# Kernel tuning notes

Hardware: AMD Instinct MI355X
Metric: run time of the kernel (lower is better)

## Reference

```python
import jax, jax.numpy as jnp
import numpy as np

N = 50000      # nodes
E = 400000     # edges
IN = 128       # in_channels
HID = 64       # hidden_channels (per head)
H = 4          # heads
OUT = 10       # classes
G = 64         # graphs in batch


def setup_inputs() -> dict:
    key = jax.random.key(0)
    ks = jax.random.split(key, 32)
    s = 0.05
    inp = {
        "x": jax.random.normal(ks[0], (N, IN), dtype=jnp.float32),
        "edge_index": jax.random.randint(ks[1], (2, E), 0, N, dtype=jnp.int32),
        "batch": jnp.sort(jax.random.randint(ks[2], (N,), 0, G, dtype=jnp.int32)),
    }
    # TransformerConv layer 1 params (in=IN -> heads*HID)
    d1 = H * HID
    inp["Wq1"] = jax.random.normal(ks[3], (IN, d1)) * s
    inp["bq1"] = jnp.zeros((d1,), jnp.float32)
    inp["Wk1"] = jax.random.normal(ks[4], (IN, d1)) * s
    inp["bk1"] = jnp.zeros((d1,), jnp.float32)
    inp["Wv1"] = jax.random.normal(ks[5], (IN, d1)) * s
    inp["bv1"] = jnp.zeros((d1,), jnp.float32)
    inp["Ws1"] = jax.random.normal(ks[6], (IN, d1)) * s   # root/skip weight
    inp["bs1"] = jnp.zeros((d1,), jnp.float32)
    # TransformerConv layer 2 params (in=H*HID -> heads*HID)
    inp["Wq2"] = jax.random.normal(ks[7], (d1, d1)) * s
    inp["bq2"] = jnp.zeros((d1,), jnp.float32)
    inp["Wk2"] = jax.random.normal(ks[8], (d1, d1)) * s
    inp["bk2"] = jnp.zeros((d1,), jnp.float32)
    inp["Wv2"] = jax.random.normal(ks[9], (d1, d1)) * s
    inp["bv2"] = jnp.zeros((d1,), jnp.float32)
    inp["Ws2"] = jax.random.normal(ks[10], (d1, d1)) * s
    inp["bs2"] = jnp.zeros((d1,), jnp.float32)
    # final classifier
    inp["Wl"] = jax.random.normal(ks[11], (d1, OUT)) * s
    inp["bl"] = jnp.zeros((OUT,), jnp.float32)
    return inp


def transformer_conv(x, src, dst, Wq, bq, Wk, bk, Wv, bv, Ws, bs):
    """PyG TransformerConv (concat=True, root_weight=True, beta=None, eval mode).
    src = edge_index[0] (source j), dst = edge_index[1] (target i).
    """
    n = x.shape[0]
    q = (x @ Wq + bq).reshape(n, H, HID)
    k = (x @ Wk + bk).reshape(n, H, HID)
    v = (x @ Wv + bv).reshape(n, H, HID)
    # per-edge attention logits [E, H]
    alpha = jnp.einsum('ehc,ehc->eh', q[dst], k[src]) / np.sqrt(HID).astype(np.float32)
    # scatter-softmax over incoming edges of each target node
    amax = jax.ops.segment_max(alpha, dst, num_segments=n)           # [N, H], -inf for isolated
    ex = jnp.exp(alpha - amax[dst])                                   # [E, H]
    denom = jax.ops.segment_sum(ex, dst, num_segments=n) + 1e-16      # [N, H]
    w = ex / denom[dst]                                               # normalized alpha [E, H]
    # scatter-sum aggregation of weighted values
    out = jax.ops.segment_sum(w[:, :, None] * v[src], dst, num_segments=n)  # [N, H, HID]
    out = out.reshape(n, H * HID)
    return out + (x @ Ws + bs)  # root/skip connection


def reference(x, edge_index, batch,
              Wq1, bq1, Wk1, bk1, Wv1, bv1, Ws1, bs1,
              Wq2, bq2, Wk2, bk2, Wv2, bv2, Ws2, bs2,
              Wl, bl):
    src, dst = edge_index[0], edge_index[1]
    h = jax.nn.elu(transformer_conv(x, src, dst, Wq1, bq1, Wk1, bk1, Wv1, bv1, Ws1, bs1))
    h = jax.nn.elu(transformer_conv(h, src, dst, Wq2, bq2, Wk2, bk2, Wv2, bv2, Ws2, bs2))
    # global mean pool per graph
    sums = jax.ops.segment_sum(h, batch, num_segments=G)              # [G, H*HID]
    cnt = jax.ops.segment_sum(jnp.ones((h.shape[0],), h.dtype), batch, num_segments=G)
    pooled = sums / jnp.maximum(cnt, 1.0)[:, None]
    logits = pooled @ Wl + bl
    return jax.nn.log_softmax(logits, axis=-1)
```

## Files before the change

### kernel.cpp

```cpp
#include <hip/hip_runtime.h>
#include <math.h>

constexpr int NN   = 50000;
constexpr int NE   = 400000;
constexpr int INC  = 128;
constexpr int NH   = 4;
constexpr int D1   = 256;
constexpr int D4   = 1024;
constexpr int NOUT = 10;
constexpr int NG   = 64;
constexpr int NB_SCAN = (NN + 255) / 256;


typedef __attribute__((ext_vector_type(8))) short bf16x8;
typedef __attribute__((ext_vector_type(4))) float f32x4;
typedef __attribute__((ext_vector_type(2))) float f32x2;

__device__ __forceinline__ short f2b(float f) {
  union { float f; unsigned int i; } v; v.f = f;
  unsigned int x = v.i;
  return (short)((x + 0x7FFFu + ((x >> 16) & 1u)) >> 16);
}
__device__ __forceinline__ float b2f(short u) {
  union { unsigned int i; float f; } v; v.i = ((unsigned int)(unsigned short)u) << 16;
  return v.f;
}
__device__ __forceinline__ float4 ld4b(const short* p) {
  short4 u = *(const short4*)p;
  return make_float4(b2f(u.x), b2f(u.y), b2f(u.z), b2f(u.w));
}
__device__ __forceinline__ int cvt_pk_bf16(float lo, float hi) {
  int r;
  asm volatile("v_cvt_pk_bf16_f32 %0, %1, %2" : "=v"(r) : "v"(lo), "v"(hi));
  return r;
}
__device__ __forceinline__ int pk_fp8x4(float a, float b, float c, float d) {
  int v = __builtin_amdgcn_cvt_pk_fp8_f32(a, b, 0, false);
  v = __builtin_amdgcn_cvt_pk_fp8_f32(c, d, v, true);
  return v;
}

__device__ __forceinline__ void gld_lds16(const short* g, short* l) {
  __builtin_amdgcn_global_load_lds(
      (const __attribute__((address_space(1))) unsigned int*)g,
      (__attribute__((address_space(3))) unsigned int*)l, 16, 0, 0);
}

constexpr int CVT_XB  = (NN * INC / 4 + 255) / 256;
constexpr int CVT_WTB = 48;
constexpr int CVT_BB  = 8;
constexpr int CVT_DB  = (NN + 255) / 256;
constexpr int CVT_FB  = 1;
constexpr int CVT_SB  = (NG * D1 + 255) / 256;

__global__ void cvt_all_k(const float* __restrict__ x, short* __restrict__ Xb,
    const float* __restrict__ Wq1, const float* __restrict__ Wk1,
    const float* __restrict__ Wv1, const float* __restrict__ Ws1,
    const float* __restrict__ Wq2, const float* __restrict__ Wk2,
    const float* __restrict__ Wv2, const float* __restrict__ Ws2,
    short* __restrict__ Wtc1, short* __restrict__ Wtc2,
    const float* __restrict__ bq1, const float* __restrict__ bk1,
    const float* __restrict__ bv1, const float* __restrict__ bs1,
    const float* __restrict__ bq2, const float* __restrict__ bk2,
    const float* __restrict__ bv2, const float* __restrict__ bs2,
    float* __restrict__ bc1, float* __restrict__ bc2,
    int* __restrict__ deg, unsigned int* __restrict__ desc,
    float* __restrict__ sums) {
  const int b = blockIdx.x;
  const int t = threadIdx.x;
  if (b < CVT_XB) {
    int i = (b * 256 + t) * 4;
    if (i >= NN * INC) return;
    float4 v = *(const float4*)(x + i);
    short4 o; o.x = f2b(v.x); o.y = f2b(v.y); o.z = f2b(v.z); o.w = f2b(v.w);
    *(short4*)(Xb + i) = o;
  } else if (b < CVT_XB + CVT_WTB) {
    const int w = b - CVT_XB;
    const bool l1 = (w < 16);
    const int mat   = l1 ? (w >> 2) : ((w - 16) >> 3);
    const int panel = l1 ? (w & 3)  : ((w - 16) & 7);
    const int K = l1 ? INC : D1;
    const int k0 = panel * 32;
    const float* Wm[8] = {Wq1, Wk1, Wv1, Ws1, Wq2, Wk2, Wv2, Ws2};
    const float* W = Wm[(l1 ? 0 : 4) + mat];
    short* Wt = l1 ? Wtc1 : Wtc2;
    int row;
    if (mat == 0)      row = t;
    else if (mat == 3) row = 768 + t;
    else               row = 256 + (t >> 2) * 8 + ((mat == 2) ? 4 : 0) + (t & 3);
    int4 pk[4];
    short* ps = (short*)pk;
#pragma unroll
    for (int kk = 0; kk < 32; ++kk)
      ps[kk] = f2b(W[(size_t)(k0 + kk) * D1 + t]);
#pragma unroll
    for (int j = 0; j < 4; ++j)
      *(int4*)(Wt + (size_t)row * K + k0 + j * 8) = pk[j];
  } else if (b < CVT_XB + CVT_WTB + CVT_BB) {
    int i = (b - CVT_XB - CVT_WTB) * 256 + t;
    if (i >= 2 * D4) return;
    int row = i & (D4 - 1);
    const float* bq = (i < D4) ? bq1 : bq2;
    const float* bk = (i < D4) ? bk1 : bk2;
    const float* bv = (i < D4) ? bv1 : bv2;
    const float* bs = (i < D4) ? bs1 : bs2;
    float v;
    if (row < 256) v = bq[row];
    else if (row < 768) {
      int j = row - 256, grp = j >> 3, off = j & 7;
      int ch = grp * 4 + (off & 3);
      v = (off < 4) ? bk[ch] : bv[ch];
    } else v = bs[row - 768];
    ((i < D4) ? bc1 : bc2)[row] = v;
  } else if (b < CVT_XB + CVT_WTB + CVT_BB + CVT_DB) {
    int i = (b - CVT_XB - CVT_WTB - CVT_BB) * 256 + t;
    if (i < NN) deg[i] = 0;
  } else if (b < CVT_XB + CVT_WTB + CVT_BB + CVT_DB + CVT_FB) {
    if (t < NB_SCAN) desc[t] = 0u;
  } else {
    int i = (b - CVT_XB - CVT_WTB - CVT_BB - CVT_DB - CVT_FB) * 256 + t;
    if (i < NG * D1) sums[i] = 0.f;
  }
}

__global__ void deg_count(const int* __restrict__ dst, int* __restrict__ deg) {
  int e = (blockIdx.x * 256 + threadIdx.x) * 4;
  if (e + 3 < NE) {
    const int4 d = *(const int4*)(dst + e);
    atomicAdd(&deg[d.x], 1);
    atomicAdd(&deg[d.y], 1);
    atomicAdd(&deg[d.z], 1);
    atomicAdd(&deg[d.w], 1);
  } else {
    for (; e < NE; ++e) atomicAdd(&deg[dst[e]], 1);
  }
}

__global__ __launch_bounds__(256) void scan_k(const int* __restrict__ deg,
    const int* __restrict__ batch, unsigned int* __restrict__ desc,
    int* __restrict__ rowstart, int* __restrict__ cursor, int* __restrict__ gb) {
  const int b = blockIdx.x;
  const int t = threadIdx.x;
  if (b == NB_SCAN) {
    if (t > NG) return;
    int lo = 0, hi = NN;
    while (lo < hi) {
      int mid = (lo + hi) >> 1;
      if (batch[mid] < t) lo = mid + 1; else hi = mid;
    }
    gb[t] = lo;
    return;
  }
  __shared__ int sh[256];
  __shared__ int base_s;
  const int i = b * 256 + t;
  const int v = (i < NN) ? deg[i] : 0;
  sh[t] = v;
  __syncthreads();
  for (int off = 1; off < 256; off <<= 1) {
    int o = (t >= off) ? sh[t - off] : 0;
    __syncthreads();
    sh[t] += o;
    __syncthreads();
  }
  const int incl = sh[t];
  const int aggr = sh[255];
  if (t == 0)
    __hip_atomic_store(&desc[b], ((unsigned int)aggr << 2) | (b == 0 ? 2u : 1u),
                       __ATOMIC_RELEASE, __HIP_MEMORY_SCOPE_AGENT);
  if (b == 0) {
    if (t == 0) base_s = 0;
  } else if (t < 64) {
    int base = 0;
    int j = b - 1;
    for (;;) {
      const int idx = j - t;
      const unsigned int d = (idx >= 0)
          ? __hip_atomic_load(&desc[idx], __ATOMIC_ACQUIRE,
                              __HIP_MEMORY_SCOPE_AGENT)
          : 2u;
      const unsigned int st = d & 3u;
      const unsigned long long m_incl = __ballot(st == 2u);
      const unsigned long long m_inv  = __ballot(st == 0u);
      const int fi = m_incl ? (__ffsll((unsigned long long)m_incl) - 1) : 64;
      const int fv = m_inv  ? (__ffsll((unsigned long long)m_inv ) - 1) : 64;
      if (fi < fv) {
        int contrib = (t <= fi) ? (int)(d >> 2) : 0;
#pragma unroll
        for (int off = 1; off < 64; off <<= 1) contrib += __shfl_xor(contrib, off, 64);
        base += contrib;
        break;
      } else if (fv == 64) {
        int contrib = (int)(d >> 2);
#pragma unroll
        for (int off = 1; off < 64; off <<= 1) contrib += __shfl_xor(contrib, off, 64);
        base += contrib;
        j -= 64;
      } else {
        __builtin_amdgcn_s_sleep(1);
      }
    }
    if (t == 0) {
      __hip_atomic_store(&desc[b], ((unsigned int)(base + aggr) << 2) | 2u,
                         __ATOMIC_RELEASE, __HIP_MEMORY_SCOPE_AGENT);
      base_s = base;
    }
  }
  __syncthreads();
  const int excl = base_s + incl - v;
  if (i <= NN) rowstart[i] = excl;
  if (i < NN)  cursor[i]   = excl;
}

__global__ void scatter_k(const int* __restrict__ src, const int* __restrict__ dst,
    int* __restrict__ cursor, int* __restrict__ esrc) {
  int e = (blockIdx.x * 256 + threadIdx.x) * 4;
  if (e + 3 < NE) {
    const int4 s4 = *(const int4*)(src + e);
    const int4 d4 = *(const int4*)(dst + e);
    esrc[atomicAdd(&cursor[d4.x], 1)] = s4.x;
    esrc[atomicAdd(&cursor[d4.y], 1)] = s4.y;
    esrc[atomicAdd(&cursor[d4.z], 1)] = s4.z;
    esrc[atomicAdd(&cursor[d4.w], 1)] = s4.w;
  } else {
    for (; e < NE; ++e) esrc[atomicAdd(&cursor[dst[e]], 1)] = src[e];
  }
}

constexpr int CLDS = 136;

__global__ __launch_bounds__(256, 4) void gemm_mfma(
    const short* __restrict__ Xb, const short* __restrict__ Wt,
    const float* __restrict__ bias, short* __restrict__ QS,
    unsigned char* __restrict__ KV8, int M, int K) {
  __shared__ short smem[24576];
  const int bx = blockIdx.x;
  const int by = blockIdx.y;
  const int m_tile = (bx & 7) + (by << 3);
  const int n_tile = bx >> 3;
  const int m0 = m_tile * 128;
  if (m0 >= M) return;
  const int n0 = n_tile * 128;

  const int t    = threadIdx.x;
  const int lane = t & 63;
  const int wv   = t >> 6;
  const int wm   = (wv >> 1) * 64;
  const int wn   = (wv & 1) * 64;
  const int quad = lane >> 4;
  const int l16  = lane & 15;
  const int lrow = lane >> 2;
  const int lseg = lane & 3;

  const int swz_w = (lseg ^ ((lrow >> 1) & 3)) * 8;
  const int swz_r = (quad ^ ((l16 >> 1) & 3)) * 8;

  auto stage = [&](int kt, int bi) {
    short* A = &smem[bi * 8192];
    short* B = &smem[bi * 8192 + 4096];
#pragma unroll
    for (int j = 0; j < 2; ++j) {
      const int rb = (wv * 2 + j) * 16;
      int gm = m0 + rb + lrow;
      gm = gm < M ? gm : M - 1;
      gld_lds16(Xb + (size_t)gm * K + kt + swz_w,               &A[rb * 32]);
      gld_lds16(Wt + (size_t)(n0 + rb + lrow) * K + kt + swz_w, &B[rb * 32]);
    }
  };

  f32x4 acc[4][4] = {};

  stage(0, 0);
  stage(32, 1);

  int bi = 0;
  for (int k0 = 0; k0 < K; k0 += 32) {
    if (k0 + 64 < K) {
      stage(k0 + 64, (bi + 2 >= 3) ? bi - 1 : bi + 2);
      asm volatile("s_waitcnt vmcnt(8)" ::: "memory");
    } else if (k0 + 32 < K) {
      asm volatile("s_waitcnt vmcnt(4)" ::: "memory");
    } else {
      asm volatile("s_waitcnt vmcnt(0)" ::: "memory");
    }
    __builtin_amdgcn_s_barrier();
    __builtin_amdgcn_sched_barrier(0);
    {
      const short* Ac = &smem[bi * 8192];
      const short* Bc = &smem[bi * 8192 + 4096];
      bf16x8 a[4], b[4];
#pragma unroll
      for (int mi = 0; mi < 4; mi++)
        a[mi] = *(const bf16x8*)(&Ac[(wm + mi * 16 + l16) * 32 + swz_r]);
#pragma unroll
      for (int nj = 0; nj < 4; nj++)
        b[nj] = *(const bf16x8*)(&Bc[(wn + nj * 16 + l16) * 32 + swz_r]);
#pragma unroll
      for (int mi = 0; mi < 4; mi++)
#pragma unroll
        for (int nj = 0; nj < 4; nj++)
          acc[mi][nj] = __builtin_amdgcn_mfma_f32_16x16x32_bf16(b[nj], a[mi], acc[mi][nj], 0, 0, 0);
    }
    __builtin_amdgcn_sched_barrier(0);
    __builtin_amdgcn_s_barrier();
    bi = (bi + 1 >= 3) ? 0 : bi + 1;
  }
  __syncthreads();

  const bool isKV = (n_tile >= 2) && (n_tile <= 5);
  float4 bz[4];
#pragma unroll
  for (int nj = 0; nj < 4; nj++)
    bz[nj] = *(const float4*)(bias + n0 + wn + nj * 16 + quad * 4);
  const int kv_base = n0 - 256;
  const int qs_base = (n_tile < 2) ? n0 : (n0 - 512);

  if (isKV) {
    unsigned char* cs = (unsigned char*)smem;
#pragma unroll
    for (int mi = 0; mi < 4; mi++) {
      const int row = wm + mi * 16 + l16;
#pragma unroll
      for (int nj = 0; nj < 4; nj++) {
        const int colb = wn + nj * 16 + quad * 4;
        const int pk = pk_fp8x4(acc[mi][nj][0] + bz[nj].x, acc[mi][nj][1] + bz[nj].y,
                                acc[mi][nj][2] + bz[nj].z, acc[mi][nj][3] + bz[nj].w);
        *(int*)(cs + row * 136 + colb) = pk;
      }
    }
    __syncthreads();
#pragma unroll
    for (int it = 0; it < 8; ++it) {
      const int chunk = it * 256 + t;
      const int row = chunk >> 4;
      const int cb  = (chunk & 15) * 8;
      const int gm  = m0 + row;
      if (gm < M)
        *(int2*)(KV8 + (size_t)gm * 512 + kv_base + cb) = *(const int2*)(cs + row * 136 + cb);
    }
  } else {
#pragma unroll
    for (int mi = 0; mi < 4; mi++) {
      const int row = wm + mi * 16 + l16;
#pragma unroll
      for (int nj = 0; nj < 4; nj++) {
        const int col = wn + nj * 16 + quad * 4;
        int2 o;
        o.x = cvt_pk_bf16(acc[mi][nj][0] + bz[nj].x, acc[mi][nj][1] + bz[nj].y);
        o.y = cvt_pk_bf16(acc[mi][nj][2] + bz[nj].z, acc[mi][nj][3] + bz[nj].w);
        *(int2*)(&smem[row * CLDS + col]) = o;
      }
    }
    __syncthreads();
#pragma unroll
    for (int it = 0; it < 8; ++it) {
      const int chunk = it * 256 + t;
      const int row = chunk >> 4;
      const int cc  = (chunk & 15) * 8;
      const int gm  = m0 + row;
      if (gm < M)
        *(int4*)(QS + (size_t)gm * 512 + qs_base + cc) = *(const int4*)(&smem[row * CLDS + cc]);
    }
  }
}

__device__ __forceinline__ f32x2 cvt_lo(int x) { return __builtin_amdgcn_cvt_pk_f32_fp8(x, false); }
__device__ __forceinline__ f32x2 cvt_hi(int x) { return __builtin_amdgcn_cvt_pk_f32_fp8(x, true); }

template <int CTRL>
__device__ __forceinline__ float ror_add(float x) {
  int y = __builtin_amdgcn_update_dpp(0, __float_as_int(x), CTRL, 0xF, 0xF, true);
  return x + __int_as_float(y);
}
__device__ __forceinline__ float red16(float x) {
  x = ror_add<0x121>(x);
  x = ror_add<0x122>(x);
  x = ror_add<0x124>(x);
  x = ror_add<0x128>(x);
  return x;
}

#define SC2 (0.125f * 1.44269504088896341f)

__device__ __forceinline__ float edge_score(const int2 x, f32x2 q01, f32x2 q23,
                                            f32x2& vv01, f32x2& vv23) {
  f32x2 kk01 = cvt_lo(x.x), kk23 = cvt_hi(x.x);
  vv01 = cvt_lo(x.y); vv23 = cvt_hi(x.y);
  f32x2 dd = q01 * kk01;
  dd += q23 * kk23;
  return red16(dd.x + dd.y);
}

template <typename TOUT>
__device__ __forceinline__ void st1(TOUT* p, float v);
template <> __device__ __forceinline__ void st1<float>(float* p, float v) { *p = v; }
template <> __device__ __forceinline__ void st1<short>(short* p, float v) { *p = f2b(v); }

template <typename TOUT>
__global__ __launch_bounds__(256) void node_attn(
    const int* __restrict__ rowstart, const int* __restrict__ esrc,
    const short* __restrict__ QS, const unsigned char* __restrict__ KV8,
    TOUT* __restrict__ out) {
  const int nid = blockIdx.x * 4 + (threadIdx.x >> 6);
  if (nid >= NN) return;
  const int t  = threadIdx.x & 63;
  const int c0 = t * 4;
  const int r0 = __builtin_amdgcn_readfirstlane(rowstart[nid]);
  const int r1 = __builtin_amdgcn_readfirstlane(rowstart[nid + 1]);
  const short4 qu = *(const short4*)(QS + (size_t)nid * 512 + c0);
  const f32x2 q01 = {b2f(qu.x) * SC2, b2f(qu.y) * SC2};
  const f32x2 q23 = {b2f(qu.z) * SC2, b2f(qu.w) * SC2};
  const unsigned char* kvb = KV8 + t * 8;
  float denom = 0.f;
  f32x2 a01 = {0.f, 0.f}, a23 = {0.f, 0.f};
  int r = r0;
  for (; r + 7 < r1; r += 8) {
    const int e0 = __builtin_amdgcn_readfirstlane(esrc[r + 0]);
    const int e1 = __builtin_amdgcn_readfirstlane(esrc[r + 1]);
    const int e2 = __builtin_amdgcn_readfirstlane(esrc[r + 2]);
    const int e3 = __builtin_amdgcn_readfirstlane(esrc[r + 3]);
    const int e4 = __builtin_amdgcn_readfirstlane(esrc[r + 4]);
    const int e5 = __builtin_amdgcn_readfirstlane(esrc[r + 5]);
    const int e6 = __builtin_amdgcn_readfirstlane(esrc[r + 6]);
    const int e7 = __builtin_amdgcn_readfirstlane(esrc[r + 7]);
    const int2 x0 = *(const int2*)(kvb + (size_t)e0 * 512);
    const int2 x1 = *(const int2*)(kvb + (size_t)e1 * 512);
    const int2 x2 = *(const int2*)(kvb + (size_t)e2 * 512);
    const int2 x3 = *(const int2*)(kvb + (size_t)e3 * 512);
    const int2 x4 = *(const int2*)(kvb + (size_t)e4 * 512);
    const int2 x5 = *(const int2*)(kvb + (size_t)e5 * 512);
    const int2 x6 = *(const int2*)(kvb + (size_t)e6 * 512);
    const int2 x7 = *(const int2*)(kvb + (size_t)e7 * 512);
    f32x2 v01_0, v23_0, v01_1, v23_1, v01_2, v23_2, v01_3, v23_3;
    f32x2 v01_4, v23_4, v01_5, v23_5, v01_6, v23_6, v01_7, v23_7;
    const float ex0 = exp2f(edge_score(x0, q01, q23, v01_0, v23_0));
    const float ex1 = exp2f(edge_score(x1, q01, q23, v01_1, v23_1));
    const float ex2 = exp2f(edge_score(x2, q01, q23, v01_2, v23_2));
    const float ex3 = exp2f(edge_score(x3, q01, q23, v01_3, v23_3));
    const float ex4 = exp2f(edge_score(x4, q01, q23, v01_4, v23_4));
    const float ex5 = exp2f(edge_score(x5, q01, q23, v01_5, v23_5));
    const float ex6 = exp2f(edge_score(x6, q01, q23, v01_6, v23_6));
    const float ex7 = exp2f(edge_score(x7, q01, q23, v01_7, v23_7));
    denom += ((ex0 + ex1) + (ex2 + ex3)) + ((ex4 + ex5) + (ex6 + ex7));
    a01 += f32x2{ex0, ex0} * v01_0; a23 += f32x2{ex0, ex0} * v23_0;
    a01 += f32x2{ex1, ex1} * v01_1; a23 += f32x2{ex1, ex1} * v23_1;
    a01 += f32x2{ex2, ex2} * v01_2; a23 += f32x2{ex2, ex2} * v23_2;
    a01 += f32x2{ex3, ex3} * v01_3; a23 += f32x2{ex3, ex3} * v23_3;
    a01 += f32x2{ex4, ex4} * v01_4; a23 += f32x2{ex4, ex4} * v23_4;
    a01 += f32x2{ex5, ex5} * v01_5; a23 += f32x2{ex5, ex5} * v23_5;
    a01 += f32x2{ex6, ex6} * v01_6; a23 += f32x2{ex6, ex6} * v23_6;
    a01 += f32x2{ex7, ex7} * v01_7; a23 += f32x2{ex7, ex7} * v23_7;
  }
  for (; r + 3 < r1; r += 4) {
    const int e0 = __builtin_amdgcn_readfirstlane(esrc[r + 0]);
    const int e1 = __builtin_amdgcn_readfirstlane(esrc[r + 1]);
    const int e2 = __builtin_amdgcn_readfirstlane(esrc[r + 2]);
    const int e3 = __builtin_amdgcn_readfirstlane(esrc[r + 3]);
    const int2 x0 = *(const int2*)(kvb + (size_t)e0 * 512);
    const int2 x1 = *(const int2*)(kvb + (size_t)e1 * 512);
    const int2 x2 = *(const int2*)(kvb + (size_t)e2 * 512);
    const int2 x3 = *(const int2*)(kvb + (size_t)e3 * 512);
    f32x2 v01_0, v23_0, v01_1, v23_1, v01_2, v23_2, v01_3, v23_3;
    const float ex0 = exp2f(edge_score(x0, q01, q23, v01_0, v23_0));
    const float ex1 = exp2f(edge_score(x1, q01, q23, v01_1, v23_1));
    const float ex2 = exp2f(edge_score(x2, q01, q23, v01_2, v23_2));
    const float ex3 = exp2f(edge_score(x3, q01, q23, v01_3, v23_3));
    denom += (ex0 + ex1) + (ex2 + ex3);
    a01 += f32x2{ex0, ex0} * v01_0; a23 += f32x2{ex0, ex0} * v23_0;
    a01 += f32x2{ex1, ex1} * v01_1; a23 += f32x2{ex1, ex1} * v23_1;
    a01 += f32x2{ex2, ex2} * v01_2; a23 += f32x2{ex2, ex2} * v23_2;
    a01 += f32x2{ex3, ex3} * v01_3; a23 += f32x2{ex3, ex3} * v23_3;
  }
  for (; r < r1; r++) {
    const int e0 = __builtin_amdgcn_readfirstlane(esrc[r]);
    const int2 x0 = *(const int2*)(kvb + (size_t)e0 * 512);
    f32x2 v01_0, v23_0;
    const float ex0 = exp2f(edge_score(x0, q01, q23, v01_0, v23_0));
    denom += ex0;
    a01 += f32x2{ex0, ex0} * v01_0; a23 += f32x2{ex0, ex0} * v23_0;
  }
  const float inv = 1.0f / (denom + 1e-16f);
  const float4 sk = ld4b(QS + (size_t)nid * 512 + 256 + c0);
  float o0 = a01.x * inv + sk.x;
  float o1 = a01.y * inv + sk.y;
  float o2 = a23.x * inv + sk.z;
  float o3 = a23.y * inv + sk.w;
  o0 = o0 > 0.f ? o0 : expm1f(o0);
  o1 = o1 > 0.f ? o1 : expm1f(o1);
  o2 = o2 > 0.f ? o2 : expm1f(o2);
  o3 = o3 > 0.f ? o3 : expm1f(o3);
  TOUT* p = out + (size_t)nid * D1 + c0;
  st1<TOUT>(p + 0, o0); st1<TOUT>(p + 1, o1);
  st1<TOUT>(p + 2, o2); st1<TOUT>(p + 3, o3);
}

__global__ __launch_bounds__(256) void pool_k(const short* __restrict__ h,
    const int* __restrict__ batch, const int* __restrict__ gb,
    float* __restrict__ sums) {
  const int c = threadIdx.x;
  const int n0 = blockIdx.x * 64;
  const int n1 = min(n0 + 64, NN);
  const int g0 = batch[n0];
  const int g1 = batch[n1 - 1];
  for (int g = g0; g <= g1; ++g) {
    const int a = max(gb[g], n0);
    const int b = min(gb[g + 1], n1);
    if (b <= a) continue;
    float s0 = 0.f, s1 = 0.f, s2 = 0.f, s3 = 0.f;
    int n = a;
    for (; n + 3 < b; n += 4) {
      s0 += b2f(h[(size_t)(n + 0) * D1 + c]);
      s1 += b2f(h[(size_t)(n + 1) * D1 + c]);
      s2 += b2f(h[(size_t)(n + 2) * D1 + c]);
      s3 += b2f(h[(size_t)(n + 3) * D1 + c]);
    }
    for (; n < b; ++n) s0 += b2f(h[(size_t)n * D1 + c]);
    atomicAdd(&sums[(size_t)g * D1 + c], (s0 + s1) + (s2 + s3));
  }
}

__global__ __launch_bounds__(640) void head_k(const float* __restrict__ sums,
    const int* __restrict__ gb, const float* __restrict__ Wl,
    const float* __restrict__ bl, float* __restrict__ out) {
  __shared__ float logits[NG][NOUT];
  const int t = threadIdx.x;
  if (t < NG * NOUT) {
    int g = t / NOUT, o = t % NOUT;
    float inv = 1.0f / fmaxf((float)(gb[g + 1] - gb[g]), 1.0f);
    float acc = 0.f;
    for (int k = 0; k < D1; k++) acc += sums[(size_t)g * D1 + k] * Wl[k * NOUT + o];
    logits[g][o] = acc * inv + bl[o];
  }
  __syncthreads();
  if (t < NG) {
    float mx = -INFINITY;
#pragma unroll
    for (int o = 0; o < NOUT; o++) mx = fmaxf(mx, logits[t][o]);
    float s = 0.f;
#pragma unroll
    for (int o = 0; o < NOUT; o++) s += __expf(logits[t][o] - mx);
    float lse = mx + logf(s);
#pragma unroll
    for (int o = 0; o < NOUT; o++) out[t * NOUT + o] = logits[t][o] - lse;
  }
}

extern "C" void kernel_launch(void* const* d_in, const int* in_sizes, int n_in,
                              void* d_out, int out_size, void* d_ws, size_t ws_size,
                              hipStream_t stream) {
  const float* x   = (const float*)d_in[0];
  const int* ei    = (const int*)d_in[1];
  const int* batch = (const int*)d_in[2];
  const float* Wq1 = (const float*)d_in[3];  const float* bq1 = (const float*)d_in[4];
  const float* Wk1 = (const float*)d_in[5];  const float* bk1 = (const float*)d_in[6];
  const float* Wv1 = (const float*)d_in[7];  const float* bv1 = (const float*)d_in[8];
  const float* Ws1 = (const float*)d_in[9];  const float* bs1 = (const float*)d_in[10];
  const float* Wq2 = (const float*)d_in[11]; const float* bq2 = (const float*)d_in[12];
  const float* Wk2 = (const float*)d_in[13]; const float* bk2 = (const float*)d_in[14];
  const float* Wv2 = (const float*)d_in[15]; const float* bv2 = (const float*)d_in[16];
  const float* Ws2 = (const float*)d_in[17]; const float* bs2 = (const float*)d_in[18];
  const float* Wl  = (const float*)d_in[19]; const float* bl  = (const float*)d_in[20];

  const int* srcIdx = ei;
  const int* dstIdx = ei + NE;

  float* ws = (float*)d_ws;
  const size_t SZ_NODE = (size_t)NN * D1;
  short* H2b  = (short*)ws;
  float* sums = ws + SZ_NODE;
  float* bc1  = sums + (size_t)NG * D1;
  float* bc2  = bc1 + D4;
  short* Xb   = (short*)(bc2 + D4);
  short* H1b  = Xb + (size_t)NN * INC;
  short* QS   = H1b + SZ_NODE;
  short* Wtc1 = QS + (size_t)NN * 512;
  short* Wtc2 = Wtc1 + (size_t)D4 * INC;
  unsigned char* KV8 = (unsigned char*)(Wtc2 + (size_t)D4 * D1);
  int* ip      = (int*)(KV8 + (size_t)NN * 512);
  int* deg     = ip;
  unsigned int* desc = (unsigned int*)(deg + NN);
  int* rowstart= (int*)(desc + 256);
  int* cursor  = rowstart + NN + 1;
  int* esrc    = cursor + NN;
  int* gb      = esrc + NE;

  const int mtiles = (NN + 127) / 128;
  const dim3 gemmGrid(64, (mtiles + 7) / 8);
  const int edgeBlocks4 = (NE / 4 + 255) / 256;
  const int aggBlocks  = (NN + 3) / 4;
  const int cvtBlocks  = CVT_XB + CVT_WTB + CVT_BB + CVT_DB + CVT_FB + CVT_SB;

  cvt_all_k<<<cvtBlocks, 256, 0, stream>>>(x, Xb,
      Wq1, Wk1, Wv1, Ws1, Wq2, Wk2, Wv2, Ws2, Wtc1, Wtc2,
      bq1, bk1, bv1, bs1, bq2, bk2, bv2, bs2, bc1, bc2, deg, desc, sums);

  deg_count<<<edgeBlocks4, 256, 0, stream>>>(dstIdx, deg);
  scan_k<<<NB_SCAN + 1, 256, 0, stream>>>(deg, batch, desc, rowstart, cursor, gb);
  scatter_k<<<edgeBlocks4, 256, 0, stream>>>(srcIdx, dstIdx, cursor, esrc);

  gemm_mfma<<<gemmGrid, 256, 0, stream>>>(Xb, Wtc1, bc1, QS, KV8, NN, INC);
  node_attn<short><<<aggBlocks, 256, 0, stream>>>(rowstart, esrc, QS, KV8, H1b);

  gemm_mfma<<<gemmGrid, 256, 0, stream>>>(H1b, Wtc2, bc2, QS, KV8, NN, D1);
  node_attn<short><<<aggBlocks, 256, 0, stream>>>(rowstart, esrc, QS, KV8, H2b);

  pool_k<<<(NN + 63) / 64, 256, 0, stream>>>(H2b, batch, gb, sums);
  head_k<<<1, 640, 0, stream>>>(sums, gb, Wl, bl, (float*)d_out);
}
```

Baseline: 328.9 us.

## Fuse CSR build into one persistent kernel and fold head into pool

Replaces the three CSR-build kernels (degree count, decoupled-lookback scan, scatter) with one 256-block persistent kernel that separates the phases with software grid barriers, using a two-level scan over per-block partials. The pool kernel also absorbs the classifier head: the last block to finish, detected with an atomic counter, computes logits and log-softmax. The aim is to cut kernel launch gaps and tail effects from small kernels. The grid barriers assume all 256 blocks are co-resident, and the edge loops use a fixed stride with fewer blocks than before.

```diff
diff --git a/kernel.cpp b/kernel.cpp
--- a/kernel.cpp
+++ b/kernel.cpp
@@ -10,6 +10,7 @@
 constexpr int NOUT = 10;
 constexpr int NG   = 64;
 constexpr int NB_SCAN = (NN + 255) / 256;
+constexpr int NB_CSR  = 256;
 
 
 typedef __attribute__((ext_vector_type(8))) short bf16x8;
@@ -44,6 +45,25 @@
   __builtin_amdgcn_global_load_lds(
       (const __attribute__((address_space(1))) unsigned int*)g,
       (__attribute__((address_space(3))) unsigned int*)l, 16, 0, 0);
+}
+
+__device__ __forceinline__ void gbar(unsigned int* cnt, unsigned int* gen, int nb) {
+  __syncthreads();
+  if (threadIdx.x == 0) {
+    const unsigned int g = __hip_atomic_load(gen, __ATOMIC_ACQUIRE,
+                                             __HIP_MEMORY_SCOPE_AGENT);
+    const unsigned int a = __hip_atomic_fetch_add(cnt, 1u, __ATOMIC_ACQ_REL,
+                                                  __HIP_MEMORY_SCOPE_AGENT);
+    if (a == (unsigned int)(nb - 1)) {
+      __hip_atomic_store(cnt, 0u, __ATOMIC_RELAXED, __HIP_MEMORY_SCOPE_AGENT);
+      __hip_atomic_fetch_add(gen, 1u, __ATOMIC_RELEASE, __HIP_MEMORY_SCOPE_AGENT);
+    } else {
+      while (__hip_atomic_load(gen, __ATOMIC_ACQUIRE,
+                               __HIP_MEMORY_SCOPE_AGENT) == g)
+        __builtin_amdgcn_s_sleep(2);
+    }
+  }
+  __syncthreads();
 }
 
 constexpr int CVT_XB  = (NN * INC / 4 + 255) / 256;
@@ -64,7 +84,7 @@
     const float* __restrict__ bq2, const float* __restrict__ bk2,
     const float* __restrict__ bv2, const float* __restrict__ bs2,
     float* __restrict__ bc1, float* __restrict__ bc2,
-    int* __restrict__ deg, unsigned int* __restrict__ desc,
+    int* __restrict__ deg, unsigned int* __restrict__ aux,
     float* __restrict__ sums) {
   const int b = blockIdx.x;
   const int t = threadIdx.x;
@@ -116,114 +136,80 @@
     int i = (b - CVT_XB - CVT_WTB - CVT_BB) * 256 + t;
     if (i < NN) deg[i] = 0;
   } else if (b < CVT_XB + CVT_WTB + CVT_BB + CVT_DB + CVT_FB) {
-    if (t < NB_SCAN) desc[t] = 0u;
+    aux[t] = 0u;
   } else {
     int i = (b - CVT_XB - CVT_WTB - CVT_BB - CVT_DB - CVT_FB) * 256 + t;
     if (i < NG * D1) sums[i] = 0.f;
   }
 }
 
-__global__ void deg_count(const int* __restrict__ dst, int* __restrict__ deg) {
-  int e = (blockIdx.x * 256 + threadIdx.x) * 4;
-  if (e + 3 < NE) {
-    const int4 d = *(const int4*)(dst + e);
-    atomicAdd(&deg[d.x], 1);
-    atomicAdd(&deg[d.y], 1);
-    atomicAdd(&deg[d.z], 1);
-    atomicAdd(&deg[d.w], 1);
-  } else {
-    for (; e < NE; ++e) atomicAdd(&deg[dst[e]], 1);
-  }
-}
-
-__global__ __launch_bounds__(256) void scan_k(const int* __restrict__ deg,
-    const int* __restrict__ batch, unsigned int* __restrict__ desc,
-    int* __restrict__ rowstart, int* __restrict__ cursor, int* __restrict__ gb) {
+__global__ __launch_bounds__(256) void csr_k(const int* __restrict__ src,
+    const int* __restrict__ dst, const int* __restrict__ batch,
+    int* __restrict__ deg, int* __restrict__ partial, unsigned int* __restrict__ bar,
+    int* __restrict__ rowstart, int* __restrict__ cursor,
+    int* __restrict__ esrc, int* __restrict__ gb) {
   const int b = blockIdx.x;
   const int t = threadIdx.x;
-  if (b == NB_SCAN) {
-    if (t > NG) return;
-    int lo = 0, hi = NN;
-    while (lo < hi) {
-      int mid = (lo + hi) >> 1;
-      if (batch[mid] < t) lo = mid + 1; else hi = mid;
-    }
-    gb[t] = lo;
-    return;
-  }
+  if (b == 255) {
+    if (t <= NG) {
+      int lo = 0, hi = NN;
+      while (lo < hi) {
+        int mid = (lo + hi) >> 1;
+        if (batch[mid] < t) lo = mid + 1; else hi = mid;
+      }
+      gb[t] = lo;
+    }
+  } else {
+    for (int e4 = b * 256 + t; e4 < NE / 4; e4 += 255 * 256) {
+      const int4 d = *(const int4*)(dst + e4 * 4);
+      atomicAdd(&deg[d.x], 1);
+      atomicAdd(&deg[d.y], 1);
+      atomicAdd(&deg[d.z], 1);
+      atomicAdd(&deg[d.w], 1);
+    }
+  }
+  gbar(&bar[0], &bar[1], NB_CSR);
   __shared__ int sh[256];
   __shared__ int base_s;
-  const int i = b * 256 + t;
-  const int v = (i < NN) ? deg[i] : 0;
-  sh[t] = v;
-  __syncthreads();
-  for (int off = 1; off < 256; off <<= 1) {
-    int o = (t >= off) ? sh[t - off] : 0;
+  int incl = 0, v = 0;
+  if (b < NB_SCAN) {
+    const int i = b * 256 + t;
+    v = (i < NN) ? deg[i] : 0;
+    sh[t] = v;
     __syncthreads();
-    sh[t] += o;
+    for (int off = 1; off < 256; off <<= 1) {
+      int o = (t >= off) ? sh[t - off] : 0;
+      __syncthreads();
+      sh[t] += o;
+      __syncthreads();
+    }
+    incl = sh[t];
+    if (t == 0) partial[b] = sh[255];
+  }
+  gbar(&bar[0], &bar[1], NB_CSR);
+  if (b < NB_SCAN) {
+    int pv = (t < b) ? partial[t] : 0;
+    sh[t] = pv;
     __syncthreads();
-  }
-  const int incl = sh[t];
-  const int aggr = sh[255];
-  if (t == 0)
-    __hip_atomic_store(&desc[b], ((unsigned int)aggr << 2) | (b == 0 ? 2u : 1u),
-                       __ATOMIC_RELEASE, __HIP_MEMORY_SCOPE_AGENT);
-  if (b == 0) {
-    if (t == 0) base_s = 0;
-  } else if (t < 64) {
-    int base = 0;
-    int j = b - 1;
-    for (;;) {
-      const int idx = j - t;
-      const unsigned int d = (idx >= 0)
-          ? __hip_atomic_load(&desc[idx], __ATOMIC_ACQUIRE,
-                              __HIP_MEMORY_SCOPE_AGENT)
-          : 2u;
-      const unsigned int st = d & 3u;
-      const unsigned long long m_incl = __ballot(st == 2u);
-      const unsigned long long m_inv  = __ballot(st == 0u);
-      const int fi = m_incl ? (__ffsll((unsigned long long)m_incl) - 1) : 64;
-      const int fv = m_inv  ? (__ffsll((unsigned long long)m_inv ) - 1) : 64;
-      if (fi < fv) {
-        int contrib = (t <= fi) ? (int)(d >> 2) : 0;
-#pragma unroll
-        for (int off = 1; off < 64; off <<= 1) contrib += __shfl_xor(contrib, off, 64);
-        base += contrib;
-        break;
-      } else if (fv == 64) {
-        int contrib = (int)(d >> 2);
-#pragma unroll
-        for (int off = 1; off < 64; off <<= 1) contrib += __shfl_xor(contrib, off, 64);
-        base += contrib;
-        j -= 64;
-      } else {
-        __builtin_amdgcn_s_sleep(1);
-      }
-    }
-    if (t == 0) {
-      __hip_atomic_store(&desc[b], ((unsigned int)(base + aggr) << 2) | 2u,
-                         __ATOMIC_RELEASE, __HIP_MEMORY_SCOPE_AGENT);
-      base_s = base;
-    }
-  }
-  __syncthreads();
-  const int excl = base_s + incl - v;
-  if (i <= NN) rowstart[i] = excl;
-  if (i < NN)  cursor[i]   = excl;
-}
-
-__global__ void scatter_k(const int* __restrict__ src, const int* __restrict__ dst,
-    int* __restrict__ cursor, int* __restrict__ esrc) {
-  int e = (blockIdx.x * 256 + threadIdx.x) * 4;
-  if (e + 3 < NE) {
-    const int4 s4 = *(const int4*)(src + e);
-    const int4 d4 = *(const int4*)(dst + e);
+    for (int off = 128; off > 0; off >>= 1) {
+      if (t < off) sh[t] += sh[t + off];
+      __syncthreads();
+    }
+    if (t == 0) base_s = sh[0];
+    __syncthreads();
+    const int i = b * 256 + t;
+    const int excl = base_s + incl - v;
+    if (i <= NN) rowstart[i] = excl;
+    if (i < NN)  cursor[i]   = excl;
+  }
+  gbar(&bar[0], &bar[1], NB_CSR);
+  for (int e4 = b * 256 + t; e4 < NE / 4; e4 += 256 * 256) {
+    const int4 s4 = *(const int4*)(src + e4 * 4);
+    const int4 d4 = *(const int4*)(dst + e4 * 4);
     esrc[atomicAdd(&cursor[d4.x], 1)] = s4.x;
     esrc[atomicAdd(&cursor[d4.y], 1)] = s4.y;
     esrc[atomicAdd(&cursor[d4.z], 1)] = s4.z;
     esrc[atomicAdd(&cursor[d4.w], 1)] = s4.w;
-  } else {
-    for (; e < NE; ++e) esrc[atomicAdd(&cursor[dst[e]], 1)] = src[e];
   }
 }
 
@@ -494,9 +480,11 @@
   st1<TOUT>(p + 2, o2); st1<TOUT>(p + 3, o3);
 }
 
-__global__ __launch_bounds__(256) void pool_k(const short* __restrict__ h,
+__global__ __launch_bounds__(256) void pool_head_k(const short* __restrict__ h,
     const int* __restrict__ batch, const int* __restrict__ gb,
-    float* __restrict__ sums) {
+    float* __restrict__ sums, unsigned int* __restrict__ done,
+    const float* __restrict__ Wl, const float* __restrict__ bl,
+    float* __restrict__ out) {
   const int c = threadIdx.x;
   const int n0 = blockIdx.x * 64;
   const int n1 = min(n0 + 64, NN);
@@ -517,31 +505,36 @@
     for (; n < b; ++n) s0 += b2f(h[(size_t)n * D1 + c]);
     atomicAdd(&sums[(size_t)g * D1 + c], (s0 + s1) + (s2 + s3));
   }
-}
-
-__global__ __launch_bounds__(640) void head_k(const float* __restrict__ sums,
-    const int* __restrict__ gb, const float* __restrict__ Wl,
-    const float* __restrict__ bl, float* __restrict__ out) {
-  __shared__ float logits[NG][NOUT];
-  const int t = threadIdx.x;
-  if (t < NG * NOUT) {
-    int g = t / NOUT, o = t % NOUT;
-    float inv = 1.0f / fmaxf((float)(gb[g + 1] - gb[g]), 1.0f);
+  __shared__ unsigned int amlast;
+  __threadfence();
+  __syncthreads();
+  if (threadIdx.x == 0) {
+    const unsigned int a = __hip_atomic_fetch_add(done, 1u, __ATOMIC_ACQ_REL,
+                                                  __HIP_MEMORY_SCOPE_AGENT);
+    amlast = (a == gridDim.x - 1) ? 1u : 0u;
+  }
+  __syncthreads();
+  if (!amlast) return;
+  __shared__ float logits[NG * NOUT];
+  for (int i = threadIdx.x; i < NG * NOUT; i += 256) {
+    const int g = i / NOUT, o = i % NOUT;
+    const float inv = 1.0f / fmaxf((float)(gb[g + 1] - gb[g]), 1.0f);
     float acc = 0.f;
     for (int k = 0; k < D1; k++) acc += sums[(size_t)g * D1 + k] * Wl[k * NOUT + o];
-    logits[g][o] = acc * inv + bl[o];
+    logits[i] = acc * inv + bl[o];
   }
   __syncthreads();
-  if (t < NG) {
+  if (threadIdx.x < NG) {
+    const int g = threadIdx.x;
     float mx = -INFINITY;
 #pragma unroll
-    for (int o = 0; o < NOUT; o++) mx = fmaxf(mx, logits[t][o]);
-    float s = 0.f;
-#pragma unroll
-    for (int o = 0; o < NOUT; o++) s += __expf(logits[t][o] - mx);
-    float lse = mx + logf(s);
-#pragma unroll
-    for (int o = 0; o < NOUT; o++) out[t * NOUT + o] = logits[t][o] - lse;
+    for (int o = 0; o < NOUT; o++) mx = fmaxf(mx, logits[g * NOUT + o]);
+    float se = 0.f;
+#pragma unroll
+    for (int o = 0; o < NOUT; o++) se += __expf(logits[g * NOUT + o] - mx);
+    const float lse = mx + logf(se);
+#pragma unroll
+    for (int o = 0; o < NOUT; o++) out[g * NOUT + o] = logits[g * NOUT + o] - lse;
   }
 }
 
@@ -578,25 +571,27 @@
   unsigned char* KV8 = (unsigned char*)(Wtc2 + (size_t)D4 * D1);
   int* ip      = (int*)(KV8 + (size_t)NN * 512);
   int* deg     = ip;
-  unsigned int* desc = (unsigned int*)(deg + NN);
-  int* rowstart= (int*)(desc + 256);
+  unsigned int* aux = (unsigned int*)(deg + NN);
+  int* partial = (int*)aux;
+  unsigned int* bar  = aux + 200;
+  unsigned int* done = aux + 204;
+  int* rowstart= (int*)(aux + 256);
   int* cursor  = rowstart + NN + 1;
   int* esrc    = cursor + NN;
   int* gb      = esrc + NE;
 
   const int mtiles = (NN + 127) / 128;
   const dim3 gemmGrid(64, (mtiles + 7) / 8);
-  const int edgeBlocks4 = (NE / 4 + 255) / 256;
   const int aggBlocks  = (NN + 3) / 4;
+  const int poolBlocks = (NN + 63) / 64;
   const int cvtBlocks  = CVT_XB + CVT_WTB + CVT_BB + CVT_DB + CVT_FB + CVT_SB;
 
   cvt_all_k<<<cvtBlocks, 256, 0, stream>>>(x, Xb,
       Wq1, Wk1, Wv1, Ws1, Wq2, Wk2, Wv2, Ws2, Wtc1, Wtc2,
-      bq1, bk1, bv1, bs1, bq2, bk2, bv2, bs2, bc1, bc2, deg, desc, sums);
-
-  deg_count<<<edgeBlocks4, 256, 0, stream>>>(dstIdx, deg);
-  scan_k<<<NB_SCAN + 1, 256, 0, stream>>>(deg, batch, desc, rowstart, cursor, gb);
-  scatter_k<<<edgeBlocks4, 256, 0, stream>>>(srcIdx, dstIdx, cursor, esrc);
+      bq1, bk1, bv1, bs1, bq2, bk2, bv2, bs2, bc1, bc2, deg, aux, sums);
+
+  csr_k<<<NB_CSR, 256, 0, stream>>>(srcIdx, dstIdx, batch, deg, partial, bar,
+                                    rowstart, cursor, esrc, gb);
 
   gemm_mfma<<<gemmGrid, 256, 0, stream>>>(Xb, Wtc1, bc1, QS, KV8, NN, INC);
   node_attn<short><<<aggBlocks, 256, 0, stream>>>(rowstart, esrc, QS, KV8, H1b);
@@ -604,6 +599,6 @@
   gemm_mfma<<<gemmGrid, 256, 0, stream>>>(H1b, Wtc2, bc2, QS, KV8, NN, D1);
   node_attn<short><<<aggBlocks, 256, 0, stream>>>(rowstart, esrc, QS, KV8, H2b);
 
-  pool_k<<<(NN + 63) / 64, 256, 0, stream>>>(H2b, batch, gb, sums);
-  head_k<<<1, 640, 0, stream>>>(sums, gb, Wl, bl, (float*)d_out);
-}
+  pool_head_k<<<poolBlocks, 256, 0, stream>>>(H2b, batch, gb, sums, done,
+                                              Wl, bl, (float*)d_out);
+}
```

Result: slower. 461.7 us (+40.4%).
